# Performance work log

Hardware: AMD Instinct MI355X
Metric: run time of the kernel (lower is better)

The kernel has to match this reference:

```python
import jax, jax.numpy as jnp
import numpy as np

C = 192; G = 12; CG = C // G          # channels, groups, channels per group
KS = 3; PAD = 1; K = KS * KS - 1      # 3x3 kernel, remove_center=True -> 8 points
HID = 4 * C                           # mlp_ratio = 4
OFFSET_SCALE = 1.0

# kernel dilation grid (x, y) pairs, center removed (remove_center=True)
_pts = np.arange(KS) - (KS - 1) // 2
_gx, _gy = np.meshgrid(_pts, _pts, indexing='ij')
_grid = np.stack([_gx.ravel(), _gy.ravel()], -1).astype(np.float32)
_grid = _grid[~np.all(_grid == 0, axis=1)]   # (K, 2)
GRID = jnp.asarray(_grid)


def _ln(x, w, b, eps=1e-5):
    mu = jnp.mean(x, -1, keepdims=True)
    var = jnp.var(x, -1, keepdims=True)
    return (x - mu) * jax.lax.rsqrt(var + eps) * w + b


def _dcnv3(x, in_proj_w, in_proj_b, dw_w, dw_b, dw_ln_w, dw_ln_b,
           off_w, off_b, mask_w, mask_b, cfs_w, cfs_b, out_proj_w, out_proj_b):
    # x: (B, H, W, C) channels-last
    B, H, W, _ = x.shape
    xp = x @ in_proj_w + in_proj_b          # value / x_proj
    # depthwise conv -> LN -> GELU on the raw input (offset/mask branch)
    x1 = jax.lax.conv_general_dilated(
        x, dw_w, (1, 1), 'SAME',
        dimension_numbers=('NHWC', 'HWIO', 'NHWC'),
        feature_group_count=C) + dw_b
    x1 = jax.nn.gelu(_ln(x1, dw_ln_w, dw_ln_b, 1e-6), approximate=False)
    off = (x1 @ off_w + off_b).reshape(B, H, W, G, K, 2)      # (dx, dy) in pixels
    mask = jax.nn.softmax((x1 @ mask_w + mask_b).reshape(B, H, W, G, K), axis=-1)
    # pad value and flatten spatial; (B, Hp*Wp, G, 1, CG)
    Hp, Wp = H + 2 * PAD, W + 2 * PAD
    v = jnp.pad(xp, ((0, 0), (PAD, PAD), (PAD, PAD), (0, 0))).reshape(B, Hp * Wp, G, 1, CG)
    # sampling locations in padded-image pixel index coords (grid_sample align_corners=False)
    bx = jnp.arange(W, dtype=x.dtype)[None, None, :, None, None] + PAD
    by = jnp.arange(H, dtype=x.dtype)[None, :, None, None, None] + PAD
    px = (bx + (GRID[:, 0] + off[..., 0]) * OFFSET_SCALE).reshape(B, H * W, G, K)
    py = (by + (GRID[:, 1] + off[..., 1]) * OFFSET_SCALE).reshape(B, H * W, G, K)
    x0 = jnp.floor(px); y0 = jnp.floor(py)
    wx = px - x0; wy = py - y0
    ix0 = x0.astype(jnp.int32); iy0 = y0.astype(jnp.int32)

    def gather(iy, ix):
        valid = ((iy >= 0) & (iy < Hp) & (ix >= 0) & (ix < Wp)).astype(x.dtype)
        idx = jnp.clip(iy, 0, Hp - 1) * Wp + jnp.clip(ix, 0, Wp - 1)
        s = jnp.take_along_axis(v, idx[..., None], axis=1)    # (B, HW, G, K, CG)
        return s * valid[..., None]

    s = (gather(iy0, ix0)         * ((1 - wy) * (1 - wx))[..., None]
       + gather(iy0, ix0 + 1)     * ((1 - wy) * wx)[..., None]
       + gather(iy0 + 1, ix0)     * (wy * (1 - wx))[..., None]
       + gather(iy0 + 1, ix0 + 1) * (wy * wx)[..., None])
    out = jnp.einsum('bngk,bngkc->bngc', mask.reshape(B, H * W, G, K), s).reshape(B, H, W, C)
    # center feature scale
    cfs = jax.nn.sigmoid(x1 @ cfs_w.T + cfs_b)                # (B, H, W, G)
    cfs = jnp.repeat(cfs, CG, axis=-1)                        # (B, H, W, C)
    out = out * (1 - cfs) + xp * cfs
    return out @ out_proj_w + out_proj_b


def _forward(x, norm1_w, norm1_b, norm2_w, norm2_b, rpn1_w, rpn1_b, rpn2_w, rpn2_b,
             in_proj_w, in_proj_b, dw_w, dw_b, dw_ln_w, dw_ln_b, off_w, off_b,
             mask_w, mask_b, cfs_w, cfs_b, out_proj_w, out_proj_b,
             fc1_w, fc1_b, fc2_w, fc2_b):
    d = _dcnv3(_ln(x, norm1_w, norm1_b), in_proj_w, in_proj_b, dw_w, dw_b,
               dw_ln_w, dw_ln_b, off_w, off_b, mask_w, mask_b, cfs_w, cfs_b,
               out_proj_w, out_proj_b)
    x = x + _ln(d, rpn1_w, rpn1_b)                            # res_post_norm branch 1
    h = jax.nn.gelu(_ln(x, norm2_w, norm2_b) @ fc1_w + fc1_b, approximate=False) @ fc2_w + fc2_b
    x = x + _ln(h, rpn2_w, rpn2_b)                            # res_post_norm branch 2
    return x


def setup_inputs():
    key = jax.random.key(0)
    ks = jax.random.split(key, 12)
    r = lambda i, shape, s=0.02: jax.random.normal(ks[i], shape, jnp.float32) * s
    B, H, W = 4, 56, 56
    return dict(
        x=jax.random.normal(ks[0], (B, H, W, C), jnp.float32),
        norm1_w=jnp.ones((C,)), norm1_b=jnp.zeros((C,)),
        norm2_w=jnp.ones((C,)), norm2_b=jnp.zeros((C,)),
        rpn1_w=jnp.ones((C,)), rpn1_b=jnp.zeros((C,)),
        rpn2_w=jnp.ones((C,)), rpn2_b=jnp.zeros((C,)),
        in_proj_w=r(1, (C, C)), in_proj_b=jnp.zeros((C,)),
        dw_w=r(2, (KS, KS, 1, C), 0.1), dw_b=jnp.zeros((C,)),
        dw_ln_w=jnp.ones((C,)), dw_ln_b=jnp.zeros((C,)),
        off_w=r(3, (C, G * K * 2), 0.1), off_b=jnp.zeros((G * K * 2,)),
        mask_w=r(4, (C, G * K), 0.1), mask_b=jnp.zeros((G * K,)),
        cfs_w=r(5, (G, C), 0.1), cfs_b=jnp.zeros((G,)),
        out_proj_w=r(6, (C, C)), out_proj_b=jnp.zeros((C,)),
        fc1_w=r(7, (C, HID)), fc1_b=jnp.zeros((HID,)),
        fc2_w=r(8, (HID, C)), fc2_b=jnp.zeros((C,)),
    )


def reference(x, norm1_w, norm1_b, norm2_w, norm2_b, rpn1_w, rpn1_b, rpn2_w, rpn2_b,
              in_proj_w, in_proj_b, dw_w, dw_b, dw_ln_w, dw_ln_b, off_w, off_b,
              mask_w, mask_b, cfs_w, cfs_b, out_proj_w, out_proj_b,
              fc1_w, fc1_b, fc2_w, fc2_b):
    return _forward(x, norm1_w, norm1_b, norm2_w, norm2_b, rpn1_w, rpn1_b, rpn2_w, rpn2_b,
                    in_proj_w, in_proj_b, dw_w, dw_b, dw_ln_w, dw_ln_b, off_w, off_b,
                    mask_w, mask_b, cfs_w, cfs_b, out_proj_w, out_proj_b,
                    fc1_w, fc1_b, fc2_w, fc2_b)
```

## Files before the change

### kernel.cpp

```cpp
#include <hip/hip_runtime.h>
#include <hip/hip_bf16.h>
#include <math.h>


#define BATCH 4
#define HH 56
#define WW 56
#define CC 192
#define NPIX (BATCH * HH * WW)
#define XS_STR 200
#define H1S 776
#define OFS 193
#define MLS 97
#define SPX 14
#define SBLK (NPIX / SPX)

typedef __hip_bfloat16 bf16;
typedef __attribute__((ext_vector_type(8))) short short8;
typedef __attribute__((ext_vector_type(4))) float float4v;

__device__ __forceinline__ float gelu_exact(float x) {
    return 0.5f * x * (1.f + erff(x * 0.70710678118654752f));
}
__device__ __forceinline__ bf16 f2b(float f) { return __float2bfloat16(f); }
__device__ __forceinline__ float b2fu(short s) {
    return __uint_as_float((unsigned)(unsigned short)s << 16);
}

__global__ __launch_bounds__(256) void prep_w_k(const float* __restrict__ inpw,
        const float* __restrict__ offw, const float* __restrict__ maskw,
        const float* __restrict__ cfsw, const float* __restrict__ outpw,
        const float* __restrict__ fc1w, const float* __restrict__ fc2w,
        bf16* __restrict__ wsB)
{
    const int i = blockIdx.x * 256 + threadIdx.x;
    bf16* inpP = wsB;
    bf16* omP  = wsB + 36864;
    bf16* outP = wsB + 95232;
    bf16* fc1P = wsB + 132096;
    bf16* fc2P = wsB + 279552;
    const int j   = i & 7;
    const int l   = (i >> 3) & 63;
    const int n15 = l & 15, q = l >> 4;
    const int grp = i >> 9;
    if (i < 36864) {
        const int t = grp / 6, c = grp - t * 6;
        const int n = 16 * t + n15, k = 32 * c + 8 * q + j;
        inpP[i] = f2b(inpw[(size_t)k * 192 + n]);
        outP[i] = f2b(outpw[(size_t)k * 192 + n]);
    }
    if (i < 58368) {
        const int t = grp / 6, c = grp - t * 6;
        const int n = 16 * t + n15, k = 32 * c + 8 * q + j;
        omP[i] = (n < 192) ? f2b(offw[(size_t)k * 192 + n])
               : (n < 288) ? f2b(maskw[(size_t)k * 96 + (n - 192)])
               : (n < 300) ? f2b(cfsw[(size_t)(n - 288) * 192 + k])
                           : f2b(0.f);
    }
    if (i < 147456) {
        const int t1 = grp / 6, c1 = grp - t1 * 6;
        const int n1 = 16 * t1 + n15, k1 = 32 * c1 + 8 * q + j;
        fc1P[i] = f2b(fc1w[(size_t)k1 * 768 + n1]);
        const int t2 = grp / 24, c2 = grp - t2 * 24;
        const int n2 = 16 * t2 + n15, k2 = 32 * c2 + 8 * q + j;
        fc2P[i] = f2b(fc2w[(size_t)k2 * 192 + n2]);
    }
}

__global__ __launch_bounds__(256) void ln_gemm8_k(const float* __restrict__ x,
        const float* __restrict__ n1w, const float* __restrict__ n1b,
        const bf16* __restrict__ wP, const float* __restrict__ bias,
        bf16* __restrict__ xn_out, bf16* __restrict__ xp_out)
{
    __shared__ __align__(16) bf16 xs[8 * XS_STR];
    const int tid = threadIdx.x;
    const int w   = tid >> 6;
    const int l   = tid & 63;
    const int n15 = l & 15;
    const int q   = l >> 4;
    const int p0  = blockIdx.x * 8;
    const int c0  = l * 4;

    #pragma unroll
    for (int rr = 0; rr < 2; rr++) {
        const int lr = 2 * w + rr;
        const int base = (p0 + lr) * CC;
        float4 v = (float4){0.f, 0.f, 0.f, 0.f};
        if (l < 48) v = *(const float4*)&x[base + c0];
        float s  = v.x + v.y + v.z + v.w;
        float qq = v.x*v.x + v.y*v.y + v.z*v.z + v.w*v.w;
        #pragma unroll
        for (int off = 32; off > 0; off >>= 1) {
            s  += __shfl_xor(s, off, 64);
            qq += __shfl_xor(qq, off, 64);
        }
        const float mu  = s * (1.f / CC);
        const float var = qq * (1.f / CC) - mu * mu;
        const float rs  = rsqrtf(var + 1e-5f);
        if (l < 48) {
            const float4 nw = *(const float4*)&n1w[c0];
            const float4 nb = *(const float4*)&n1b[c0];
            ushort4 u;
            bf16 h;
            h = f2b((v.x - mu) * rs * nw.x + nb.x); u.x = *(unsigned short*)&h;
            h = f2b((v.y - mu) * rs * nw.y + nb.y); u.y = *(unsigned short*)&h;
            h = f2b((v.z - mu) * rs * nw.z + nb.z); u.z = *(unsigned short*)&h;
            h = f2b((v.w - mu) * rs * nw.w + nb.w); u.w = *(unsigned short*)&h;
            *(ushort4*)&xs[lr * XS_STR + c0] = u;
            *(ushort4*)&xn_out[base + c0] = u;
        }
    }
    __syncthreads();

    short8 aF[6];
    #pragma unroll
    for (int c = 0; c < 6; c++)
        aF[c] = (n15 < 8)
              ? *(const short8*)&xs[n15 * XS_STR + c * 32 + q * 8]
              : (short8){0, 0, 0, 0, 0, 0, 0, 0};

    for (int t = w; t < 12; t += 4) {
        float4v acc = (float4v){0.f, 0.f, 0.f, 0.f};
        #pragma unroll
        for (int c = 0; c < 6; c++) {
            const short8 bF = *(const short8*)&wP[(size_t)((t * 6 + c) * 64 + l) * 8];
            acc = __builtin_amdgcn_mfma_f32_16x16x32_bf16(aF[c], bF, acc, 0, 0, 0);
        }
        if (q < 2) {
            const int n0 = 16 * t;
            const float bb = bias[n0 + n15];
            #pragma unroll
            for (int r = 0; r < 4; r++)
                xp_out[(size_t)(p0 + 4 * q + r) * 192 + n0 + n15] = f2b(acc[r] + bb);
        }
    }
}

__global__ __launch_bounds__(256) void sample_mlp_k(
        const bf16* __restrict__ xp, const bf16* __restrict__ xn,
        const float* __restrict__ dww, const float* __restrict__ dwb,
        const float* __restrict__ dwlnw, const float* __restrict__ dwlnb,
        const bf16* __restrict__ omP, const float* __restrict__ offb,
        const float* __restrict__ maskb, const float* __restrict__ cfsb,
        const bf16* __restrict__ wP, const float* __restrict__ bias,
        const float* __restrict__ x,
        const float* __restrict__ r1w, const float* __restrict__ r1b,
        const float* __restrict__ n2w, const float* __restrict__ n2b,
        const bf16* __restrict__ fc1P, const float* __restrict__ fc1b,
        const bf16* __restrict__ fc2P, const float* __restrict__ fc2b,
        const float* __restrict__ r2w, const float* __restrict__ r2b,
        float* __restrict__ out)
{
    __shared__ __align__(16) bf16 xs[16 * XS_STR];
    __shared__ __align__(16) char uni[16 * H1S * 2];
    __shared__ float ps[4][16], pq[4][16], ps2[4][16], pq2[4][16];

    float (*cv)[192]     = (float(*)[192])uni;
    float (*offs_l)[OFS] = (float(*)[OFS])uni;
    float (*mls_l)[MLS]  = (float(*)[MLS])(uni + 12352);
    float (*cfs_l)[16]   = (float(*)[16])(uni + 18560);
    bf16* h1             = (bf16*)uni;

    const int tid = threadIdx.x;
    const int w   = tid >> 6;
    const int l   = tid & 63;
    const int n15 = l & 15;
    const int q   = l >> 4;
    const int bid = (blockIdx.x & 7) * (SBLK / 8) + (blockIdx.x >> 3);
    const int p0  = bid * SPX;

    if (tid < SPX * 12) {
        const int px  = tid / 12;
        const int ch0 = (tid - px * 12) * 16;
        const int pix = p0 + px;
        const int bimg = pix / (HH * WW);
        const int hw   = pix - bimg * (HH * WW);
        const int h    = hw / WW;
        const int wx   = hw - h * WW;
        const int ibase = bimg * (HH * WW * CC);

        float a[16];
        #pragma unroll
        for (int j = 0; j < 16; j += 4) {
            const float4 b4 = *(const float4*)&dwb[ch0 + j];
            a[j] = b4.x; a[j+1] = b4.y; a[j+2] = b4.z; a[j+3] = b4.w;
        }
        #pragma unroll
        for (int ky = 0; ky < 3; ky++) {
            const int yy = h + ky - 1;
            if (yy < 0 || yy >= HH) continue;
            #pragma unroll
            for (int kx = 0; kx < 3; kx++) {
                const int xx = wx + kx - 1;
                if (xx < 0 || xx >= WW) continue;
                const int o = ibase + (yy * WW + xx) * CC + ch0;
                const short8 v0 = *(const short8*)&xn[o];
                const short8 v1 = *(const short8*)&xn[o + 8];
                const int wo = (ky * 3 + kx) * CC + ch0;
                const float4 w0 = *(const float4*)&dww[wo];
                const float4 w1 = *(const float4*)&dww[wo + 4];
                const float4 w2 = *(const float4*)&dww[wo + 8];
                const float4 w3 = *(const float4*)&dww[wo + 12];
                a[0]  += b2fu(v0[0]) * w0.x; a[1]  += b2fu(v0[1]) * w0.y;
                a[2]  += b2fu(v0[2]) * w0.z; a[3]  += b2fu(v0[3]) * w0.w;
                a[4]  += b2fu(v0[4]) * w1.x; a[5]  += b2fu(v0[5]) * w1.y;
                a[6]  += b2fu(v0[6]) * w1.z; a[7]  += b2fu(v0[7]) * w1.w;
                a[8]  += b2fu(v1[0]) * w2.x; a[9]  += b2fu(v1[1]) * w2.y;
                a[10] += b2fu(v1[2]) * w2.z; a[11] += b2fu(v1[3]) * w2.w;
                a[12] += b2fu(v1[4]) * w3.x; a[13] += b2fu(v1[5]) * w3.y;
                a[14] += b2fu(v1[6]) * w3.z; a[15] += b2fu(v1[7]) * w3.w;
            }
        }
        #pragma unroll
        for (int j = 0; j < 16; j += 4)
            *(float4*)&cv[px][ch0 + j] = (float4){a[j], a[j+1], a[j+2], a[j+3]};
    }
    __syncthreads();

    #pragma unroll
    for (int pass = 0; pass < 4; pass++) {
        const int px = w + 4 * pass;
        if (px >= SPX) break;
        float v[3];
        #pragma unroll
        for (int i = 0; i < 3; i++) v[i] = cv[px][l + 64 * i];
        float s = v[0] + v[1] + v[2];
        float qq = v[0]*v[0] + v[1]*v[1] + v[2]*v[2];
        #pragma unroll
        for (int off = 32; off > 0; off >>= 1) {
            s  += __shfl_xor(s, off, 64);
            qq += __shfl_xor(qq, off, 64);
        }
        const float mu  = s * (1.f / CC);
        const float var = qq * (1.f / CC) - mu * mu;
        const float rs  = rsqrtf(var + 1e-6f);
        #pragma unroll
        for (int i = 0; i < 3; i++) {
            const int c = l + 64 * i;
            xs[px * XS_STR + c] = f2b(gelu_exact((v[i] - mu) * rs * dwlnw[c] + dwlnb[c]));
        }
    }
    __syncthreads();

    {
        short8 aF[6];
        #pragma unroll
        for (int c = 0; c < 6; c++)
            aF[c] = *(const short8*)&xs[n15 * XS_STR + c * 32 + q * 8];

        for (int t = w; t < 19; t += 4) {
            float4v acc = (float4v){0.f, 0.f, 0.f, 0.f};
            #pragma unroll
            for (int c = 0; c < 6; c++) {
                const short8 bF = *(const short8*)&omP[(size_t)((t * 6 + c) * 64 + l) * 8];
                acc = __builtin_amdgcn_mfma_f32_16x16x32_bf16(aF[c], bF, acc, 0, 0, 0);
            }
            if (t < 12) {
                const int n0 = 16 * t;
                const float bb = offb[n0 + n15];
                #pragma unroll
                for (int r = 0; r < 4; r++)
                    offs_l[4 * q + r][n0 + n15] = acc[r] + bb;
            } else if (t < 18) {
                const int m0 = 16 * t - 192;
                const float bb = maskb[m0 + n15];
                #pragma unroll
                for (int r = 0; r < 4; r++) {
                    const float vv = acc[r] + bb;
                    float mx = vv;
                    mx = fmaxf(mx, __shfl_xor(mx, 1, 64));
                    mx = fmaxf(mx, __shfl_xor(mx, 2, 64));
                    mx = fmaxf(mx, __shfl_xor(mx, 4, 64));
                    const float e = __expf(vv - mx);
                    float se = e;
                    se += __shfl_xor(se, 1, 64);
                    se += __shfl_xor(se, 2, 64);
                    se += __shfl_xor(se, 4, 64);
                    mls_l[4 * q + r][m0 + n15] = e * (1.f / se);
                }
            } else {
                const float bb = (n15 < 12) ? cfsb[n15] : 0.f;
                #pragma unroll
                for (int r = 0; r < 4; r++) {
                    const float cf = 1.f / (1.f + __expf(-(acc[r] + bb)));
                    if (n15 < 12) cfs_l[4 * q + r][n15] = cf;
                }
            }
        }
    }
    __syncthreads();

    if (tid < SPX * 12) {
        const int px  = tid / 12;
        const int g   = tid - px * 12;
        const int ch0 = g * 16;
        const int pix = p0 + px;
        const int bimg = pix / (HH * WW);
        const int hw   = pix - bimg * (HH * WW);
        const int h    = hw / WW;
        const int wxp  = hw - h * WW;
        const int ibase = bimg * (HH * WW * CC);

        const float cf = cfs_l[px][g];

        float acc[16];
        #pragma unroll
        for (int j = 0; j < 16; j++) acc[j] = 0.f;

        #pragma unroll 2
        for (int k = 0; k < 8; k++) {
            const int kk = k + (k >= 4 ? 1 : 0);
            const int gx = kk / 3 - 1;
            const int gy = kk - (kk / 3) * 3 - 1;
            const float mk  = mls_l[px][g * 8 + k];
            const float px_ = (float)(wxp + gx) + offs_l[px][g * 16 + 2 * k];
            const float py_ = (float)(h   + gy) + offs_l[px][g * 16 + 2 * k + 1];
            const float fx = floorf(px_), fy = floorf(py_);
            const float wxf = px_ - fx, wyf = py_ - fy;
            const int x0 = (int)fx, y0 = (int)fy;
            const float vx0 = ((unsigned)x0       < WW) ? 1.f : 0.f;
            const float vx1 = ((unsigned)(x0 + 1) < WW) ? 1.f : 0.f;
            const float vy0 = ((unsigned)y0       < HH) ? 1.f : 0.f;
            const float vy1 = ((unsigned)(y0 + 1) < HH) ? 1.f : 0.f;
            const int x0c = min(max(x0, 0), WW - 1);
            const int x1c = min(max(x0 + 1, 0), WW - 1);
            const int y0c = min(max(y0, 0), HH - 1);
            const int y1c = min(max(y0 + 1, 0), HH - 1);
            const float wx0 = (1.f - wxf) * vx0, wx1 = wxf * vx1;
            const float wy0 = (1.f - wyf) * vy0, wy1 = wyf * vy1;
            const float w00 = mk * wy0 * wx0, w01 = mk * wy0 * wx1;
            const float w10 = mk * wy1 * wx0, w11 = mk * wy1 * wx1;
            const int r0 = ibase + y0c * (WW * CC) + ch0;
            const int r1 = ibase + y1c * (WW * CC) + ch0;
            const int o00 = r0 + x0c * CC, o01 = r0 + x1c * CC;
            const int o10 = r1 + x0c * CC, o11 = r1 + x1c * CC;
            const short8 a00 = *(const short8*)&xp[o00];
            const short8 b00 = *(const short8*)&xp[o00 + 8];
            const short8 a01 = *(const short8*)&xp[o01];
            const short8 b01 = *(const short8*)&xp[o01 + 8];
            const short8 a10 = *(const short8*)&xp[o10];
            const short8 b10 = *(const short8*)&xp[o10 + 8];
            const short8 a11 = *(const short8*)&xp[o11];
            const short8 b11 = *(const short8*)&xp[o11 + 8];
            #pragma unroll
            for (int j = 0; j < 8; j++) {
                acc[j]     += w00 * b2fu(a00[j]) + w01 * b2fu(a01[j])
                            + w10 * b2fu(a10[j]) + w11 * b2fu(a11[j]);
                acc[8 + j] += w00 * b2fu(b00[j]) + w01 * b2fu(b01[j])
                            + w10 * b2fu(b10[j]) + w11 * b2fu(b11[j]);
            }
        }

        const int po = pix * CC + ch0;
        const short8 xv0 = *(const short8*)&xp[po];
        const short8 xv1 = *(const short8*)&xp[po + 8];
        short8 o0, o1;
        #pragma unroll
        for (int j = 0; j < 8; j++) {
            const float v0 = acc[j]     * (1.f - cf) + b2fu(xv0[j]) * cf;
            const float v1 = acc[8 + j] * (1.f - cf) + b2fu(xv1[j]) * cf;
            bf16 hh;
            hh = f2b(v0); o0[j] = *(short*)&hh;
            hh = f2b(v1); o1[j] = *(short*)&hh;
        }
        *(short8*)&xs[px * XS_STR + ch0]     = o0;
        *(short8*)&xs[px * XS_STR + ch0 + 8] = o1;
    }
    __syncthreads();

    {
        short8 aF[6];
        #pragma unroll
        for (int c = 0; c < 6; c++)
            aF[c] = *(const short8*)&xs[n15 * XS_STR + c * 32 + q * 8];

        float4v acc[3];
        #pragma unroll
        for (int t = 0; t < 3; t++) {
            const int tile = 3 * w + t;
            acc[t] = (float4v){0.f, 0.f, 0.f, 0.f};
            #pragma unroll
            for (int c = 0; c < 6; c++) {
                const short8 bF = *(const short8*)&wP[(size_t)((tile * 6 + c) * 64 + l) * 8];
                acc[t] = __builtin_amdgcn_mfma_f32_16x16x32_bf16(aF[c], bF, acc[t], 0, 0, 0);
            }
            const float bb = bias[16 * tile + n15];
            #pragma unroll
            for (int r = 0; r < 4; r++) acc[t][r] += bb;
        }

        #pragma unroll
        for (int r = 0; r < 4; r++) {
            float sp = acc[0][r] + acc[1][r] + acc[2][r];
            float qp = acc[0][r]*acc[0][r] + acc[1][r]*acc[1][r] + acc[2][r]*acc[2][r];
            #pragma unroll
            for (int o = 1; o < 16; o <<= 1) {
                sp += __shfl_xor(sp, o, 64);
                qp += __shfl_xor(qp, o, 64);
            }
            if (n15 == 0) { ps[w][4 * q + r] = sp; pq[w][4 * q + r] = qp; }
        }
        __syncthreads();

        float x2v[3][4];
        #pragma unroll
        for (int r = 0; r < 4; r++) {
            const int row = 4 * q + r;
            const float s  = ps[0][row] + ps[1][row] + ps[2][row] + ps[3][row];
            const float qq = pq[0][row] + pq[1][row] + pq[2][row] + pq[3][row];
            const float mu  = s * (1.f / CC);
            const float var = qq * (1.f / CC) - mu * mu;
            const float rs  = rsqrtf(var + 1e-5f);
            const int growc = min(p0 + row, NPIX - 1);
            #pragma unroll
            for (int t = 0; t < 3; t++) {
                const int col = 48 * w + 16 * t + n15;
                x2v[t][r] = x[(size_t)growc * CC + col] + (acc[t][r] - mu) * rs * r1w[col] + r1b[col];
            }
        }
        #pragma unroll
        for (int r = 0; r < 4; r++) {
            float sp = x2v[0][r] + x2v[1][r] + x2v[2][r];
            float qp = x2v[0][r]*x2v[0][r] + x2v[1][r]*x2v[1][r] + x2v[2][r]*x2v[2][r];
            #pragma unroll
            for (int o = 1; o < 16; o <<= 1) {
                sp += __shfl_xor(sp, o, 64);
                qp += __shfl_xor(qp, o, 64);
            }
            if (n15 == 0) { ps2[w][4 * q + r] = sp; pq2[w][4 * q + r] = qp; }
        }
        __syncthreads();

        #pragma unroll
        for (int r = 0; r < 4; r++) {
            const int row = 4 * q + r;
            const float s  = ps2[0][row] + ps2[1][row] + ps2[2][row] + ps2[3][row];
            const float qq = pq2[0][row] + pq2[1][row] + pq2[2][row] + pq2[3][row];
            const float mu  = s * (1.f / CC);
            const float var = qq * (1.f / CC) - mu * mu;
            const float rs  = rsqrtf(var + 1e-5f);
            #pragma unroll
            for (int t = 0; t < 3; t++) {
                const int col = 48 * w + 16 * t + n15;
                xs[row * XS_STR + col] = f2b((x2v[t][r] - mu) * rs * n2w[col] + n2b[col]);
            }
        }
        __syncthreads();

        short8 aF2[6];
        #pragma unroll
        for (int c = 0; c < 6; c++)
            aF2[c] = *(const short8*)&xs[n15 * XS_STR + c * 32 + q * 8];

        #pragma unroll
        for (int t1 = 0; t1 < 12; t1++) {
            const int tile = 12 * w + t1;
            float4v a1 = (float4v){0.f, 0.f, 0.f, 0.f};
            #pragma unroll
            for (int c = 0; c < 6; c++) {
                const short8 bF = *(const short8*)&fc1P[(size_t)((tile * 6 + c) * 64 + l) * 8];
                a1 = __builtin_amdgcn_mfma_f32_16x16x32_bf16(aF2[c], bF, a1, 0, 0, 0);
            }
            const int n0 = 16 * tile;
            const float bb = fc1b[n0 + n15];
            #pragma unroll
            for (int r = 0; r < 4; r++)
                h1[(4 * q + r) * H1S + n0 + n15] = f2b(gelu_exact(a1[r] + bb));
        }
        __syncthreads();

        float4v acc2[3];
        #pragma unroll
        for (int t = 0; t < 3; t++) acc2[t] = (float4v){0.f, 0.f, 0.f, 0.f};
        #pragma unroll 4
        for (int kc = 0; kc < 24; kc++) {
            const short8 a2 = *(const short8*)&h1[n15 * H1S + kc * 32 + q * 8];
            #pragma unroll
            for (int t = 0; t < 3; t++) {
                const int tile = 3 * w + t;
                const short8 bF = *(const short8*)&fc2P[(size_t)((tile * 24 + kc) * 64 + l) * 8];
                acc2[t] = __builtin_amdgcn_mfma_f32_16x16x32_bf16(a2, bF, acc2[t], 0, 0, 0);
            }
        }
        #pragma unroll
        for (int t = 0; t < 3; t++) {
            const float bb = fc2b[48 * w + 16 * t + n15];
            #pragma unroll
            for (int r = 0; r < 4; r++) acc2[t][r] += bb;
        }

        #pragma unroll
        for (int r = 0; r < 4; r++) {
            float sp = acc2[0][r] + acc2[1][r] + acc2[2][r];
            float qp = acc2[0][r]*acc2[0][r] + acc2[1][r]*acc2[1][r] + acc2[2][r]*acc2[2][r];
            #pragma unroll
            for (int o = 1; o < 16; o <<= 1) {
                sp += __shfl_xor(sp, o, 64);
                qp += __shfl_xor(qp, o, 64);
            }
            if (n15 == 0) { ps[w][4 * q + r] = sp; pq[w][4 * q + r] = qp; }
        }
        __syncthreads();

        #pragma unroll
        for (int r = 0; r < 4; r++) {
            const int row = 4 * q + r;
            if (row >= SPX) continue;
            const float s  = ps[0][row] + ps[1][row] + ps[2][row] + ps[3][row];
            const float qq = pq[0][row] + pq[1][row] + pq[2][row] + pq[3][row];
            const float mu  = s * (1.f / CC);
            const float var = qq * (1.f / CC) - mu * mu;
            const float rs  = rsqrtf(var + 1e-5f);
            const size_t grow = p0 + row;
            #pragma unroll
            for (int t = 0; t < 3; t++) {
                const int col = 48 * w + 16 * t + n15;
                out[grow * CC + col] = x2v[t][r]
                                     + (acc2[t][r] - mu) * rs * r2w[col] + r2b[col];
            }
        }
    }
}

extern "C" void kernel_launch(void* const* d_in, const int* in_sizes, int n_in,
                              void* d_out, int out_size, void* d_ws, size_t ws_size,
                              hipStream_t stream) {
    const float* x      = (const float*)d_in[0];
    const float* n1w    = (const float*)d_in[1];
    const float* n1b    = (const float*)d_in[2];
    const float* n2w    = (const float*)d_in[3];
    const float* n2b    = (const float*)d_in[4];
    const float* rpn1w  = (const float*)d_in[5];
    const float* rpn1b  = (const float*)d_in[6];
    const float* rpn2w  = (const float*)d_in[7];
    const float* rpn2b  = (const float*)d_in[8];
    const float* inpw   = (const float*)d_in[9];
    const float* inpb   = (const float*)d_in[10];
    const float* dww    = (const float*)d_in[11];
    const float* dwb    = (const float*)d_in[12];
    const float* dwlnw  = (const float*)d_in[13];
    const float* dwlnb  = (const float*)d_in[14];
    const float* offw   = (const float*)d_in[15];
    const float* offb   = (const float*)d_in[16];
    const float* maskw  = (const float*)d_in[17];
    const float* maskb  = (const float*)d_in[18];
    const float* cfsw   = (const float*)d_in[19];
    const float* cfsb   = (const float*)d_in[20];
    const float* outpw  = (const float*)d_in[21];
    const float* outpb  = (const float*)d_in[22];
    const float* fc1w   = (const float*)d_in[23];
    const float* fc1b   = (const float*)d_in[24];
    const float* fc2w   = (const float*)d_in[25];
    const float* fc2b   = (const float*)d_in[26];

    const int N = NPIX;
    const size_t NP = (size_t)N * CC;
    bf16* B0  = (bf16*)d_ws;
    bf16* B1  = B0 + NP;
    bf16* wsB = B1 + NP;
    const bf16* inpP = wsB;
    const bf16* omP  = wsB + 36864;
    const bf16* outP = wsB + 95232;
    const bf16* fc1P = wsB + 132096;
    const bf16* fc2P = wsB + 279552;

    prep_w_k<<<576, 256, 0, stream>>>(inpw, offw, maskw, cfsw, outpw, fc1w, fc2w, wsB);
    ln_gemm8_k<<<N / 8, 256, 0, stream>>>(x, n1w, n1b, inpP, inpb, B0, B1);
    sample_mlp_k<<<SBLK, 256, 0, stream>>>(B1, B0, dww, dwb, dwlnw, dwlnb,
                                           omP, offb, maskb, cfsb,
                                           outP, outpb, x, rpn1w, rpn1b,
                                           n2w, n2b, fc1P, fc1b, fc2P, fc2b,
                                           rpn2w, rpn2b, (float*)d_out);
}
```

Before: 180.1 us.

## Stage xp output through LDS for vector stores and prefetch residual loads early

In ln_gemm8_k, the GEMM results are staged in a shared buffer and then written to global memory as 16-byte row stores, replacing scattered 2-byte stores. In sample_mlp_k, the residual x values and the center-pixel xp values are loaded at kernel start so their latency overlaps the depthwise conv and sampling stages. The cv shared-memory row stride is padded from 192 to 196 to reduce bank conflicts. In exchange, register pressure rises from holding the prefetched values, and there is extra shared memory plus a barrier.

```diff
diff --git a/kernel.cpp b/kernel.cpp
--- a/kernel.cpp
+++ b/kernel.cpp
@@ -12,6 +12,7 @@
 #define H1S 776
 #define OFS 193
 #define MLS 97
+#define CVS 196
 #define SPX 14
 #define SBLK (NPIX / SPX)
 
@@ -73,6 +74,7 @@
         bf16* __restrict__ xn_out, bf16* __restrict__ xp_out)
 {
     __shared__ __align__(16) bf16 xs[8 * XS_STR];
+    __shared__ __align__(16) bf16 xs2[8 * XS_STR];
     const int tid = threadIdx.x;
     const int w   = tid >> 6;
     const int l   = tid & 63;
@@ -131,8 +133,15 @@
             const float bb = bias[n0 + n15];
             #pragma unroll
             for (int r = 0; r < 4; r++)
-                xp_out[(size_t)(p0 + 4 * q + r) * 192 + n0 + n15] = f2b(acc[r] + bb);
-        }
+                xs2[(4 * q + r) * XS_STR + n0 + n15] = f2b(acc[r] + bb);
+        }
+    }
+    __syncthreads();
+
+    if (tid < 192) {
+        const int row = tid / 24, c8 = tid - row * 24;
+        *(short8*)&xp_out[(size_t)(p0 + row) * CC + c8 * 8] =
+            *(const short8*)&xs2[row * XS_STR + c8 * 8];
     }
 }
 
@@ -155,7 +164,7 @@
     __shared__ __align__(16) char uni[16 * H1S * 2];
     __shared__ float ps[4][16], pq[4][16], ps2[4][16], pq2[4][16];
 
-    float (*cv)[192]     = (float(*)[192])uni;
+    float (*cv)[CVS]     = (float(*)[CVS])uni;
     float (*offs_l)[OFS] = (float(*)[OFS])uni;
     float (*mls_l)[MLS]  = (float(*)[MLS])(uni + 12352);
     float (*cfs_l)[16]   = (float(*)[16])(uni + 18560);
@@ -169,34 +178,50 @@
     const int bid = (blockIdx.x & 7) * (SBLK / 8) + (blockIdx.x >> 3);
     const int p0  = bid * SPX;
 
-    if (tid < SPX * 12) {
-        const int px  = tid / 12;
-        const int ch0 = (tid - px * 12) * 16;
-        const int pix = p0 + px;
-        const int bimg = pix / (HH * WW);
-        const int hw   = pix - bimg * (HH * WW);
-        const int h    = hw / WW;
-        const int wx   = hw - h * WW;
-        const int ibase = bimg * (HH * WW * CC);
-
+    float xpre[3][4];
+    #pragma unroll
+    for (int r = 0; r < 4; r++) {
+        const int growc = min(p0 + 4 * q + r, NPIX - 1);
+        #pragma unroll
+        for (int t = 0; t < 3; t++)
+            xpre[t][r] = x[(size_t)growc * CC + 48 * w + 16 * t + n15];
+    }
+    const bool samp = tid < SPX * 12;
+    const int s_px  = tid / 12;
+    const int s_g   = tid - s_px * 12;
+    const int s_ch0 = s_g * 16;
+    const int s_pix = min(p0 + s_px, NPIX - 1);
+    const int s_bim = s_pix / (HH * WW);
+    const int s_hw  = s_pix - s_bim * (HH * WW);
+    const int s_h   = s_hw / WW;
+    const int s_wxp = s_hw - s_h * WW;
+    const int s_ib  = s_bim * (HH * WW * CC);
+    short8 xv0p = {0,0,0,0,0,0,0,0}, xv1p = {0,0,0,0,0,0,0,0};
+    if (samp) {
+        const int po = s_pix * CC + s_ch0;
+        xv0p = *(const short8*)&xp[po];
+        xv1p = *(const short8*)&xp[po + 8];
+    }
+
+    if (samp) {
         float a[16];
         #pragma unroll
         for (int j = 0; j < 16; j += 4) {
-            const float4 b4 = *(const float4*)&dwb[ch0 + j];
+            const float4 b4 = *(const float4*)&dwb[s_ch0 + j];
             a[j] = b4.x; a[j+1] = b4.y; a[j+2] = b4.z; a[j+3] = b4.w;
         }
         #pragma unroll
         for (int ky = 0; ky < 3; ky++) {
-            const int yy = h + ky - 1;
+            const int yy = s_h + ky - 1;
             if (yy < 0 || yy >= HH) continue;
             #pragma unroll
             for (int kx = 0; kx < 3; kx++) {
-                const int xx = wx + kx - 1;
+                const int xx = s_wxp + kx - 1;
                 if (xx < 0 || xx >= WW) continue;
-                const int o = ibase + (yy * WW + xx) * CC + ch0;
+                const int o = s_ib + (yy * WW + xx) * CC + s_ch0;
                 const short8 v0 = *(const short8*)&xn[o];
                 const short8 v1 = *(const short8*)&xn[o + 8];
-                const int wo = (ky * 3 + kx) * CC + ch0;
+                const int wo = (ky * 3 + kx) * CC + s_ch0;
                 const float4 w0 = *(const float4*)&dww[wo];
                 const float4 w1 = *(const float4*)&dww[wo + 4];
                 const float4 w2 = *(const float4*)&dww[wo + 8];
@@ -213,7 +238,7 @@
         }
         #pragma unroll
         for (int j = 0; j < 16; j += 4)
-            *(float4*)&cv[px][ch0 + j] = (float4){a[j], a[j+1], a[j+2], a[j+3]};
+            *(float4*)&cv[s_px][s_ch0 + j] = (float4){a[j], a[j+1], a[j+2], a[j+3]};
     }
     __syncthreads();
 
@@ -290,18 +315,8 @@
     }
     __syncthreads();
 
-    if (tid < SPX * 12) {
-        const int px  = tid / 12;
-        const int g   = tid - px * 12;
-        const int ch0 = g * 16;
-        const int pix = p0 + px;
-        const int bimg = pix / (HH * WW);
-        const int hw   = pix - bimg * (HH * WW);
-        const int h    = hw / WW;
-        const int wxp  = hw - h * WW;
-        const int ibase = bimg * (HH * WW * CC);
-
-        const float cf = cfs_l[px][g];
+    if (samp) {
+        const float cf = cfs_l[s_px][s_g];
 
         float acc[16];
         #pragma unroll
@@ -312,9 +327,9 @@
             const int kk = k + (k >= 4 ? 1 : 0);
             const int gx = kk / 3 - 1;
             const int gy = kk - (kk / 3) * 3 - 1;
-            const float mk  = mls_l[px][g * 8 + k];
-            const float px_ = (float)(wxp + gx) + offs_l[px][g * 16 + 2 * k];
-            const float py_ = (float)(h   + gy) + offs_l[px][g * 16 + 2 * k + 1];
+            const float mk  = mls_l[s_px][s_g * 8 + k];
+            const float px_ = (float)(s_wxp + gx) + offs_l[s_px][s_g * 16 + 2 * k];
+            const float py_ = (float)(s_h   + gy) + offs_l[s_px][s_g * 16 + 2 * k + 1];
             const float fx = floorf(px_), fy = floorf(py_);
             const float wxf = px_ - fx, wyf = py_ - fy;
             const int x0 = (int)fx, y0 = (int)fy;
@@ -330,8 +345,8 @@
             const float wy0 = (1.f - wyf) * vy0, wy1 = wyf * vy1;
             const float w00 = mk * wy0 * wx0, w01 = mk * wy0 * wx1;
             const float w10 = mk * wy1 * wx0, w11 = mk * wy1 * wx1;
-            const int r0 = ibase + y0c * (WW * CC) + ch0;
-            const int r1 = ibase + y1c * (WW * CC) + ch0;
+            const int r0 = s_ib + y0c * (WW * CC) + s_ch0;
+            const int r1 = s_ib + y1c * (WW * CC) + s_ch0;
             const int o00 = r0 + x0c * CC, o01 = r0 + x1c * CC;
             const int o10 = r1 + x0c * CC, o11 = r1 + x1c * CC;
             const short8 a00 = *(const short8*)&xp[o00];
@@ -351,20 +366,17 @@
             }
         }
 
-        const int po = pix * CC + ch0;
-        const short8 xv0 = *(const short8*)&xp[po];
-        const short8 xv1 = *(const short8*)&xp[po + 8];
         short8 o0, o1;
         #pragma unroll
         for (int j = 0; j < 8; j++) {
-            const float v0 = acc[j]     * (1.f - cf) + b2fu(xv0[j]) * cf;
-            const float v1 = acc[8 + j] * (1.f - cf) + b2fu(xv1[j]) * cf;
+            const float v0 = acc[j]     * (1.f - cf) + b2fu(xv0p[j]) * cf;
+            const float v1 = acc[8 + j] * (1.f - cf) + b2fu(xv1p[j]) * cf;
             bf16 hh;
             hh = f2b(v0); o0[j] = *(short*)&hh;
             hh = f2b(v1); o1[j] = *(short*)&hh;
         }
-        *(short8*)&xs[px * XS_STR + ch0]     = o0;
-        *(short8*)&xs[px * XS_STR + ch0 + 8] = o1;
+        *(short8*)&xs[s_px * XS_STR + s_ch0]     = o0;
+        *(short8*)&xs[s_px * XS_STR + s_ch0 + 8] = o1;
     }
     __syncthreads();
 
@@ -411,11 +423,10 @@
             const float mu  = s * (1.f / CC);
             const float var = qq * (1.f / CC) - mu * mu;
             const float rs  = rsqrtf(var + 1e-5f);
-            const int growc = min(p0 + row, NPIX - 1);
             #pragma unroll
             for (int t = 0; t < 3; t++) {
                 const int col = 48 * w + 16 * t + n15;
-                x2v[t][r] = x[(size_t)growc * CC + col] + (acc[t][r] - mu) * rs * r1w[col] + r1b[col];
+                x2v[t][r] = xpre[t][r] + (acc[t][r] - mu) * rs * r1w[col] + r1b[col];
             }
         }
         #pragma unroll
```

Result: slower. 185.4 us (+3.0%).
